# Kernel tuning notes

Hardware: AMD Instinct MI355X
Metric: run time of the kernel (lower is better)

## Reference

```python
import jax, jax.numpy as jnp
import numpy as np

D = 1024
H = 16
HD = D // H
B = 2
S = 2048


def setup_inputs() -> dict:
    key = jax.random.key(0)
    ks = jax.random.split(key, 9)
    sc = 1.0 / np.sqrt(D)
    return {
        "x": jax.random.normal(ks[0], (B, S, D), dtype=jnp.float32),
        "attention_mask": jnp.ones((B, S), dtype=jnp.int32),
        "Wq": jax.random.normal(ks[1], (D, D), dtype=jnp.float32) * sc,
        "bq": jax.random.normal(ks[2], (D,), dtype=jnp.float32) * 0.02,
        "Wk": jax.random.normal(ks[3], (D, D), dtype=jnp.float32) * sc,
        "bk": jax.random.normal(ks[4], (D,), dtype=jnp.float32) * 0.02,
        "Wv": jax.random.normal(ks[5], (D, D), dtype=jnp.float32) * sc,
        "bv": jax.random.normal(ks[6], (D,), dtype=jnp.float32) * 0.02,
        "Wo": jax.random.normal(ks[7], (D, D), dtype=jnp.float32) * sc,
        "bo": jax.random.normal(ks[8], (D,), dtype=jnp.float32) * 0.02,
    }


def reference(x, attention_mask, Wq, bq, Wk, bk, Wv, bv, Wo, bo):
    Bb, Ss, d = x.shape
    # projections (torch Linear: x @ W.T + b; here W stored as [in,out])
    q = (x @ Wq + bq).reshape(Bb, Ss, H, HD).transpose(0, 2, 1, 3)  # [B,H,S,hd]
    k = (x @ Wk + bk).reshape(Bb, Ss, H, HD).transpose(0, 2, 1, 3)
    v = (x @ Wv + bv).reshape(Bb, Ss, H, HD).transpose(0, 2, 1, 3)
    dots = jnp.einsum("bhqd,bhkd->bhqk", q, k) / np.sqrt(HD)  # [B,H,S,S]
    causal = jnp.triu(jnp.ones((Ss, Ss), dtype=bool), k=1)  # True above diagonal
    dots = jnp.where(causal[None, None], -jnp.inf, dots)
    pad = (attention_mask == 0)[:, None, None, :]  # [B,1,1,S]
    dots = jnp.where(pad, -jnp.inf, dots)
    scores = jax.nn.softmax(dots, axis=-1)
    o = jnp.einsum("bhqk,bhkd->bhqd", scores, v)  # [B,H,S,hd]
    o = o.transpose(0, 2, 1, 3).reshape(Bb, Ss, d)
    return o @ Wo + bo
```

## Files before the change

### kernel.cpp

```cpp
#include <hip/hip_runtime.h>

#define D_  1024
#define H_  16
#define HD_ 64
#define B_  2
#define S_  2048
#define M_  (B_*S_)

typedef _Float16 f16;
typedef _Float16 f16x8 __attribute__((ext_vector_type(8)));
typedef _Float16 f16x4 __attribute__((ext_vector_type(4)));
typedef _Float16 f16x2 __attribute__((ext_vector_type(2)));
typedef float    f32x4 __attribute__((ext_vector_type(4)));

#define GLOAD_LDS16(g, l) \
  __builtin_amdgcn_global_load_lds((__attribute__((address_space(1))) const void*)(g), \
                                   (__attribute__((address_space(3))) void*)(l), 16, 0, 0)

__global__ void k_cvt_x(const float* __restrict__ x, f16* __restrict__ xb) {
  int i = blockIdx.x * blockDim.x + threadIdx.x;
  float4 v = ((const float4*)x)[i];
  f16x4 o = { (f16)v.x, (f16)v.y, (f16)v.z, (f16)v.w };
  ((f16x4*)xb)[i] = o;
}

__global__ void k_twt(const float* __restrict__ W, f16* __restrict__ WT) {
  __shared__ float t[32][33];
  int n0 = blockIdx.x * 32, k0 = blockIdx.y * 32;
  int tx = threadIdx.x, ty = threadIdx.y;
  #pragma unroll
  for (int i = 0; i < 4; i++)
    t[ty + i*8][tx] = W[(size_t)(k0 + ty + i*8) * D_ + n0 + tx];
  __syncthreads();
  #pragma unroll
  for (int i = 0; i < 4; i++)
    WT[(size_t)(n0 + ty + i*8) * D_ + k0 + tx] = (f16)t[tx][ty + i*8];
}

template<int MODE>
__device__ __forceinline__ void gemm_body(const f16* __restrict__ A,
                                          const f16* __restrict__ Bt,
                                          const float* __restrict__ bias,
                                          void* __restrict__ Cout) {
  __shared__ __align__(16) f16 lA[128 * 32];
  __shared__ __align__(16) f16 lB[128 * 32];
  const int tid = threadIdx.x;
  const int wv = tid >> 6, lane = tid & 63;
  const int m0 = blockIdx.y * 128, n0 = blockIdx.x * 128;
  const int fr = lane & 15, fg = lane >> 4;
  const int wm = wv >> 1, wn = wv & 1;
  f32x4 acc[4][4] = {};

  for (int k0 = 0; k0 < D_; k0 += 32) {
    #pragma unroll
    for (int it = 0; it < 2; ++it) {
      int c = wv + it * 4;
      int row = c * 16 + (lane >> 2);
      int kk = (lane & 3) * 8;
      GLOAD_LDS16(A  + (size_t)(m0 + row) * D_ + k0 + kk, lA + c * 512);
      GLOAD_LDS16(Bt + (size_t)(n0 + row) * D_ + k0 + kk, lB + c * 512);
    }
    __syncthreads();
    f16x8 a[4], b[4];
    #pragma unroll
    for (int i = 0; i < 4; i++) a[i] = *(const f16x8*)&lA[(wm*64 + i*16 + fr) * 32 + fg * 8];
    #pragma unroll
    for (int j = 0; j < 4; j++) b[j] = *(const f16x8*)&lB[(wn*64 + j*16 + fr) * 32 + fg * 8];
    #pragma unroll
    for (int i = 0; i < 4; i++)
      #pragma unroll
      for (int j = 0; j < 4; j++)
        acc[i][j] = __builtin_amdgcn_mfma_f32_16x16x32_f16(a[i], b[j], acc[i][j], 0, 0, 0);
    __syncthreads();
  }

  #pragma unroll
  for (int i = 0; i < 4; i++) {
    #pragma unroll
    for (int j = 0; j < 4; j++) {
      int grow0 = m0 + wm*64 + i*16 + fg*4;
      int gcol  = n0 + wn*64 + j*16 + fr;
      float bb = bias[gcol];
      #pragma unroll
      for (int r = 0; r < 4; r++) {
        float val = acc[i][j][r] + bb;
        int grow = grow0 + r;
        if (MODE == 0) {
          int b = grow >> 11, s = grow & (S_ - 1);
          int h = gcol >> 6,  hd = gcol & (HD_ - 1);
          ((f16*)Cout)[((size_t)(b * H_ + h) * S_ + s) * HD_ + hd] = (f16)val;
        } else {
          ((float*)Cout)[(size_t)grow * D_ + gcol] = val;
        }
      }
    }
  }
}

__global__ __launch_bounds__(256) void k_gemm_qkv(const f16* __restrict__ A,
                                                  const f16* __restrict__ WT0,
                                                  const float* __restrict__ bq,
                                                  const float* __restrict__ bk,
                                                  const float* __restrict__ bv,
                                                  f16* __restrict__ qkv) {
  int z = blockIdx.z;
  const f16* Bt = WT0 + (size_t)z * D_ * D_;
  const float* bias = (z == 0) ? bq : (z == 1) ? bk : bv;
  f16* outp = qkv + (size_t)z * M_ * D_;
  gemm_body<0>(A, Bt, bias, outp);
}

__global__ __launch_bounds__(256) void k_gemm_out(const f16* __restrict__ A,
                                                  const f16* __restrict__ Bt,
                                                  const float* __restrict__ bias,
                                                  float* __restrict__ Cout) {
  gemm_body<1>(A, Bt, bias, Cout);
}

#define POFF 8.65617025f

__global__ __launch_bounds__(256) void k_attn(const f16* __restrict__ Qh,
                                              const f16* __restrict__ Kh,
                                              const f16* __restrict__ Vh,
                                              const int* __restrict__ am,
                                              f16* __restrict__ OpA, f16* __restrict__ OpB,
                                              float* __restrict__ lpA, float* __restrict__ lpB) {
  __shared__ __align__(16) f16 kt[2][64 * 64];
  __shared__ __align__(16) f16 vt[2][64 * 64];
  __shared__ __align__(16) f16 pl[4][32 * 64];

  const int tid = threadIdx.x;
  const int wv = tid >> 6, lane = tid & 63;
  const int fr = lane & 15, fg = lane >> 4;

  const int d = blockIdx.x;
  const int bh = d & 31;
  const int m  = (d >> 5) & 7;
  const int typeB = d >> 8;
  const int b = bh >> 4, h = bh & 15;
  (void)h;

  f16*   Op = typeB ? OpB : OpA;
  float* lp = typeB ? lpB : lpA;

  const f16* Qb = Qh + (size_t)bh * S_ * HD_;
  const f16* Kb = Kh + (size_t)bh * S_ * HD_;
  const f16* Vb = Vh + (size_t)bh * S_ * HD_;
  const int* amb = am + b * S_;
  f16* plw = pl[wv];

  volatile int* flag = (volatile int*)&pl[0][0];
  if (tid == 0) *flag = 1;
  __syncthreads();
  {
    int mv = 1;
    #pragma unroll
    for (int i = 0; i < 8; ++i) mv &= amb[tid * 8 + i];
    if (!mv) *flag = 0;
  }
  __syncthreads();
  const bool allv = (*flag != 0);

  const f16 qs = (f16)0.18033688f;
  const int ksrc = 8 * ((lane & 7) ^ (lane >> 3));
  const int swz = (fr & 7) << 3;
  const int vkk = (tid >> 3) * 2, vd0 = (tid & 7) * 8;
  const int vswz2 = (tid & 3) << 4;
  const f32x4 cinit = { -POFF, -POFF, -POFF, -POFF };

#define STAGE_K(t_, c_) do { \
    const f16* kp_ = Kb + (size_t)((t_) * 64) * HD_; \
    GLOAD_LDS16(kp_ + (size_t)((wv*2+0)*8 + (lane >> 3)) * HD_ + ksrc, &kt[c_][(wv*2+0)*512]); \
    GLOAD_LDS16(kp_ + (size_t)((wv*2+1)*8 + (lane >> 3)) * HD_ + ksrc, &kt[c_][(wv*2+1)*512]); \
  } while (0)

#define LOAD_V(t_) do { \
    const f16* vp_ = Vb + (size_t)((t_) * 64 + vkk) * HD_ + vd0; \
    vA = *(const f16x8*)vp_; vBr = *(const f16x8*)(vp_ + HD_); \
  } while (0)

#define WRITE_V(c_) do { \
    _Pragma("unroll") \
    for (int j_ = 0; j_ < 8; ++j_) { \
      f16x2 pr_ = { vA[j_], vBr[j_] }; \
      *(f16x2*)&vt[c_][(vd0 + j_) * 64 + ((vkk ^ (j_ << 3)) ^ vswz2)] = pr_; \
    } \
  } while (0)

  f16x8 vA, vBr;

  auto run_half = [&](int qt, int t0, int t1) {
    const int q0w = qt * 128 + wv * 32;

    f16x8 qf[2][2];
    #pragma unroll
    for (int rt = 0; rt < 2; ++rt) {
      f16x8 r0 = *(const f16x8*)&Qb[(size_t)(q0w + rt*16 + fr) * HD_ + fg*8];
      f16x8 r1 = *(const f16x8*)&Qb[(size_t)(q0w + rt*16 + fr) * HD_ + 32 + fg*8];
      qf[rt][0] = r0 * qs; qf[rt][1] = r1 * qs;
    }

    f32x4 accO[2][4] = {};
    float lrl[2] = {0.f, 0.f};

    STAGE_K(t0, 0);
    LOAD_V(t0);
    WRITE_V(0);
    __syncthreads();

    int c = 0;
    for (int t = t0; t < t1; ++t) {
      const int kb = t * 64;
      const bool pre = (t + 1 < t1);
      if (pre) { STAGE_K(t + 1, c ^ 1); LOAD_V(t + 1); }

      const int dq = q0w - kb;
      if (dq + 31 >= 0) {
        int tm1 = (dq + 31) >> 4; if (tm1 > 3) tm1 = 3;
        int tm0 = (dq + 15) >> 4; if (tm0 > 3) tm0 = 3;
        const bool fullb = (dq >= 63);

        f32x4 s[2][4];
        #pragma unroll
        for (int rt = 0; rt < 2; ++rt)
          #pragma unroll
          for (int tt = 0; tt < 4; ++tt) s[rt][tt] = cinit;

        __builtin_amdgcn_s_setprio(1);
        #pragma unroll
        for (int tt = 0; tt < 4; ++tt) {
          if (tt <= tm1) {
            const int kr = (tt*16 + fr) * 64;
            f16x8 kf0 = *(const f16x8*)&kt[c][kr + ((     fg*8) ^ swz)];
            f16x8 kf1 = *(const f16x8*)&kt[c][kr + ((32 + fg*8) ^ swz)];
            s[1][tt] = __builtin_amdgcn_mfma_f32_16x16x32_f16(kf0, qf[1][0], s[1][tt], 0, 0, 0);
            s[1][tt] = __builtin_amdgcn_mfma_f32_16x16x32_f16(kf1, qf[1][1], s[1][tt], 0, 0, 0);
            if (tt <= tm0) {
              s[0][tt] = __builtin_amdgcn_mfma_f32_16x16x32_f16(kf0, qf[0][0], s[0][tt], 0, 0, 0);
              s[0][tt] = __builtin_amdgcn_mfma_f32_16x16x32_f16(kf1, qf[0][1], s[0][tt], 0, 0, 0);
            }
          }
        }
        __builtin_amdgcn_s_setprio(0);

        #pragma unroll
        for (int rt = 0; rt < 2; ++rt) {
          const int tmr = rt ? tm1 : tm0;
          if (tmr < 0) continue;
          const int thr = dq + rt*16 + fr;
          #pragma unroll
          for (int tt = 0; tt < 4; ++tt) {
            f16x4 pk4 = {};
            if (tt <= tmr) {
              if (allv) {
                #pragma unroll
                for (int r = 0; r < 4; ++r) {
                  float sv = s[rt][tt][r];
                  if (!fullb) sv = (tt*16 + fg*4 + r <= thr) ? sv : -1e30f;
                  float p = exp2f(sv);
                  lrl[rt] += p;
                  pk4[r] = (f16)p;
                }
              } else {
                int4 a4 = *(const int4*)&amb[kb + tt*16 + fg*4];
                #pragma unroll
                for (int r = 0; r < 4; ++r) {
                  float sv = s[rt][tt][r];
                  if (!fullb) sv = (tt*16 + fg*4 + r <= thr) ? sv : -1e30f;
                  float p = exp2f(sv);
                  int mr_ = (r == 0) ? a4.x : (r == 1) ? a4.y : (r == 2) ? a4.z : a4.w;
                  p = mr_ ? p : 0.0f;
                  lrl[rt] += p;
                  pk4[r] = (f16)p;
                }
              }
            }
            *(f16x4*)&plw[(rt*16 + fr) * 64 + ((tt*16 + fg*4) ^ swz)] = pk4;
          }
        }

        __builtin_amdgcn_s_setprio(1);
        #pragma unroll
        for (int ks = 0; ks < 2; ++ks) {
          if (ks <= (tm1 >> 1)) {
            f16x8 vf[4];
            #pragma unroll
            for (int nt = 0; nt < 4; ++nt)
              vf[nt] = *(const f16x8*)&vt[c][(nt*16 + fr) * 64 +
                           ((ks*32 + fg*8) ^ swz ^ (((2*nt + (fr >> 3)) & 3) << 4))];
            #pragma unroll
            for (int rt = 0; rt < 2; ++rt) {
              const int tmr = rt ? tm1 : tm0;
              if (tmr >= 0 && ks <= (tmr >> 1)) {
                f16x8 pa = *(const f16x8*)&plw[(rt*16 + fr) * 64 + ((ks*32 + fg*8) ^ swz)];
                #pragma unroll
                for (int nt = 0; nt < 4; ++nt)
                  accO[rt][nt] = __builtin_amdgcn_mfma_f32_16x16x32_f16(pa, vf[nt], accO[rt][nt], 0, 0, 0);
              }
            }
          }
        }
        __builtin_amdgcn_s_setprio(0);
      }

      if (pre) WRITE_V(c ^ 1);
      __syncthreads();
      c ^= 1;
    }

    #pragma unroll
    for (int rt = 0; rt < 2; ++rt) {
      float v = lrl[rt];
      v += __shfl_xor(v, 16);
      v += __shfl_xor(v, 32);
      if (lane < 16) lp[(size_t)bh * S_ + q0w + rt*16 + lane] = v;

      float inv[4];
      (void)inv;
      f16* Oprow = Op + (size_t)bh * (S_ * HD_);
      #pragma unroll
      for (int nt = 0; nt < 4; ++nt) {
        int col = nt*16 + fr;
        #pragma unroll
        for (int r = 0; r < 4; ++r) {
          int row = q0w + rt*16 + fg*4 + r;
          Oprow[(size_t)row * HD_ + col] = (f16)accO[rt][nt][r];
        }
      }
    }
  };

  const int qtA = m, qtB = 15 - m;
  if (!typeB) {
    run_half(qtA, 0, qtA + 1);
    run_half(qtB, 0, qtB + 1);
  } else {
    run_half(qtA, qtA + 1, 2 * (qtA + 1));
    run_half(qtB, qtB + 1, 2 * (qtB + 1));
  }

#undef STAGE_K
#undef LOAD_V
#undef WRITE_V
}

__global__ __launch_bounds__(256) void k_comb(const f16* __restrict__ OA,
                                              const f16* __restrict__ OB,
                                              const float* __restrict__ lA,
                                              const float* __restrict__ lB,
                                              f16* __restrict__ Obf) {
  int gid = blockIdx.x * 256 + threadIdx.x;
  int seg = gid & 7, rowg = gid >> 3;
  int bh = rowg >> 11, row = rowg & 2047;
  f16x8 a  = ((const f16x8*)OA)[gid];
  f16x8 b2 = ((const f16x8*)OB)[gid];
  float inv = __builtin_amdgcn_rcpf(lA[rowg] + lB[rowg]);
  f16x8 o;
  #pragma unroll
  for (int j = 0; j < 8; ++j) o[j] = (f16)(((float)a[j] + (float)b2[j]) * inv);
  int bb = bh >> 4, hh = bh & 15;
  *(f16x8*)&Obf[((size_t)(bb * S_ + row)) * D_ + hh * 64 + seg * 8] = o;
}

extern "C" void kernel_launch(void* const* d_in, const int* in_sizes, int n_in,
                              void* d_out, int out_size, void* d_ws, size_t ws_size,
                              hipStream_t stream) {
  const float* x  = (const float*)d_in[0];
  const int*   am = (const int*)d_in[1];
  const float* Wq = (const float*)d_in[2];
  const float* bq = (const float*)d_in[3];
  const float* Wk = (const float*)d_in[4];
  const float* bk = (const float*)d_in[5];
  const float* Wv = (const float*)d_in[6];
  const float* bv = (const float*)d_in[7];
  const float* Wo = (const float*)d_in[8];
  const float* bo = (const float*)d_in[9];

  char* ws = (char*)d_ws;
  f16*   xb  = (f16*)(ws);
  f16*   wt  = (f16*)(ws + (8u  << 20));
  f16*   qkv = (f16*)(ws + (16u << 20));
  f16*   OpA = (f16*)(ws + (40u << 20));
  f16*   OpB = xb;
  float* lpA = (float*)(ws + (8u << 20));
  float* lpB = (float*)(ws + (8u << 20) + (256u << 10));
  f16*   Obf = qkv;

  k_cvt_x<<<4096, 256, 0, stream>>>(x, xb);

  dim3 tb(32, 8), tg(32, 32);
  k_twt<<<tg, tb, 0, stream>>>(Wq, wt + 0 * (size_t)(D_ * D_));
  k_twt<<<tg, tb, 0, stream>>>(Wk, wt + 1 * (size_t)(D_ * D_));
  k_twt<<<tg, tb, 0, stream>>>(Wv, wt + 2 * (size_t)(D_ * D_));
  k_twt<<<tg, tb, 0, stream>>>(Wo, wt + 3 * (size_t)(D_ * D_));

  k_gemm_qkv<<<dim3(8, 32, 3), 256, 0, stream>>>(xb, wt, bq, bk, bv, qkv);

  k_attn<<<dim3(512), 256, 0, stream>>>(qkv,
                                        qkv + (size_t)M_ * D_,
                                        qkv + 2 * (size_t)M_ * D_,
                                        am, OpA, OpB, lpA, lpB);

  k_comb<<<dim3(2048), 256, 0, stream>>>(OpA, OpB, lpA, lpB, Obf);

  k_gemm_out<<<dim3(8, 32), 256, 0, stream>>>(Obf, wt + 3 * (size_t)(D_ * D_), bo,
                                              (float*)d_out);
}
```

Before: 132.6 us.

## Double-buffer GEMM LDS, merge weight transposes, compute softmax row sums via MFMA

After: 124.6 us. 6.0% less time.

```diff
diff --git a/kernel.cpp b/kernel.cpp
--- a/kernel.cpp
+++ b/kernel.cpp
@@ -11,6 +11,7 @@
 typedef _Float16 f16x8 __attribute__((ext_vector_type(8)));
 typedef _Float16 f16x4 __attribute__((ext_vector_type(4)));
 typedef _Float16 f16x2 __attribute__((ext_vector_type(2)));
+typedef __fp16   h16x2 __attribute__((ext_vector_type(2)));
 typedef float    f32x4 __attribute__((ext_vector_type(4)));
 
 #define GLOAD_LDS16(g, l) \
@@ -24,8 +25,13 @@
   ((f16x4*)xb)[i] = o;
 }
 
-__global__ void k_twt(const float* __restrict__ W, f16* __restrict__ WT) {
+__global__ void k_twt4(const float* __restrict__ Wq, const float* __restrict__ Wk,
+                       const float* __restrict__ Wv, const float* __restrict__ Wo,
+                       f16* __restrict__ WT) {
   __shared__ float t[32][33];
+  int z = blockIdx.z;
+  const float* W = (z == 0) ? Wq : (z == 1) ? Wk : (z == 2) ? Wv : Wo;
+  f16* out = WT + (size_t)z * D_ * D_;
   int n0 = blockIdx.x * 32, k0 = blockIdx.y * 32;
   int tx = threadIdx.x, ty = threadIdx.y;
   #pragma unroll
@@ -34,7 +40,7 @@
   __syncthreads();
   #pragma unroll
   for (int i = 0; i < 4; i++)
-    WT[(size_t)(n0 + ty + i*8) * D_ + k0 + tx] = (f16)t[tx][ty + i*8];
+    out[(size_t)(n0 + ty + i*8) * D_ + k0 + tx] = (f16)t[tx][ty + i*8];
 }
 
 template<int MODE>
@@ -42,37 +48,46 @@
                                           const f16* __restrict__ Bt,
                                           const float* __restrict__ bias,
                                           void* __restrict__ Cout) {
-  __shared__ __align__(16) f16 lA[128 * 32];
-  __shared__ __align__(16) f16 lB[128 * 32];
+  __shared__ __align__(16) f16 lA[2][128 * 32];
+  __shared__ __align__(16) f16 lB[2][128 * 32];
   const int tid = threadIdx.x;
   const int wv = tid >> 6, lane = tid & 63;
   const int m0 = blockIdx.y * 128, n0 = blockIdx.x * 128;
   const int fr = lane & 15, fg = lane >> 4;
   const int wm = wv >> 1, wn = wv & 1;
+  const int srow = (lane >> 2), skk = (lane & 3) * 8;
   f32x4 acc[4][4] = {};
 
+#define G_STAGE(k0_, c_) do { \
+    _Pragma("unroll") \
+    for (int it_ = 0; it_ < 2; ++it_) { \
+      int ch_ = wv + it_ * 4; \
+      int row_ = ch_ * 16 + srow; \
+      GLOAD_LDS16(A  + (size_t)(m0 + row_) * D_ + (k0_) + skk, &lA[c_][ch_ * 512]); \
+      GLOAD_LDS16(Bt + (size_t)(n0 + row_) * D_ + (k0_) + skk, &lB[c_][ch_ * 512]); \
+    } \
+  } while (0)
+
+  G_STAGE(0, 0);
+  __syncthreads();
+
+  int c = 0;
   for (int k0 = 0; k0 < D_; k0 += 32) {
-    #pragma unroll
-    for (int it = 0; it < 2; ++it) {
-      int c = wv + it * 4;
-      int row = c * 16 + (lane >> 2);
-      int kk = (lane & 3) * 8;
-      GLOAD_LDS16(A  + (size_t)(m0 + row) * D_ + k0 + kk, lA + c * 512);
-      GLOAD_LDS16(Bt + (size_t)(n0 + row) * D_ + k0 + kk, lB + c * 512);
-    }
-    __syncthreads();
+    if (k0 + 32 < D_) G_STAGE(k0 + 32, c ^ 1);
     f16x8 a[4], b[4];
     #pragma unroll
-    for (int i = 0; i < 4; i++) a[i] = *(const f16x8*)&lA[(wm*64 + i*16 + fr) * 32 + fg * 8];
-    #pragma unroll
-    for (int j = 0; j < 4; j++) b[j] = *(const f16x8*)&lB[(wn*64 + j*16 + fr) * 32 + fg * 8];
+    for (int i = 0; i < 4; i++) a[i] = *(const f16x8*)&lA[c][(wm*64 + i*16 + fr) * 32 + fg * 8];
+    #pragma unroll
+    for (int j = 0; j < 4; j++) b[j] = *(const f16x8*)&lB[c][(wn*64 + j*16 + fr) * 32 + fg * 8];
     #pragma unroll
     for (int i = 0; i < 4; i++)
       #pragma unroll
       for (int j = 0; j < 4; j++)
         acc[i][j] = __builtin_amdgcn_mfma_f32_16x16x32_f16(a[i], b[j], acc[i][j], 0, 0, 0);
     __syncthreads();
+    c ^= 1;
   }
+#undef G_STAGE
 
   #pragma unroll
   for (int i = 0; i < 4; i++) {
@@ -80,15 +95,17 @@
     for (int j = 0; j < 4; j++) {
       int grow0 = m0 + wm*64 + i*16 + fg*4;
       int gcol  = n0 + wn*64 + j*16 + fr;
-      float bb = bias[gcol];
+      float bb = bias[gcol & (D_ - 1)];
       #pragma unroll
       for (int r = 0; r < 4; r++) {
         float val = acc[i][j][r] + bb;
         int grow = grow0 + r;
         if (MODE == 0) {
+          int z = gcol >> 10, gl = gcol & (D_ - 1);
           int b = grow >> 11, s = grow & (S_ - 1);
-          int h = gcol >> 6,  hd = gcol & (HD_ - 1);
-          ((f16*)Cout)[((size_t)(b * H_ + h) * S_ + s) * HD_ + hd] = (f16)val;
+          int h = gl >> 6,  hd = gl & (HD_ - 1);
+          ((f16*)Cout)[(size_t)z * (M_ * D_) +
+                       ((size_t)(b * H_ + h) * S_ + s) * HD_ + hd] = (f16)val;
         } else {
           ((float*)Cout)[(size_t)grow * D_ + gcol] = val;
         }
@@ -103,11 +120,9 @@
                                                   const float* __restrict__ bk,
                                                   const float* __restrict__ bv,
                                                   f16* __restrict__ qkv) {
-  int z = blockIdx.z;
-  const f16* Bt = WT0 + (size_t)z * D_ * D_;
-  const float* bias = (z == 0) ? bq : (z == 1) ? bk : bv;
-  f16* outp = qkv + (size_t)z * M_ * D_;
-  gemm_body<0>(A, Bt, bias, outp);
+  const int n0 = blockIdx.x * 128;
+  const float* bias = (n0 < 1024) ? bq : (n0 < 2048) ? bk : bv;
+  gemm_body<0>(A, WT0, bias, qkv);
 }
 
 __global__ __launch_bounds__(256) void k_gemm_out(const f16* __restrict__ A,
@@ -167,6 +182,8 @@
   const int vkk = (tid >> 3) * 2, vd0 = (tid & 7) * 8;
   const int vswz2 = (tid & 3) << 4;
   const f32x4 cinit = { -POFF, -POFF, -POFF, -POFF };
+  const f16 one_ = (f16)1.0f;
+  const f16x8 onesf = { one_, one_, one_, one_, one_, one_, one_, one_ };
 
 #define STAGE_K(t_, c_) do { \
     const f16* kp_ = Kb + (size_t)((t_) * 64) * HD_; \
@@ -201,7 +218,7 @@
     }
 
     f32x4 accO[2][4] = {};
-    float lrl[2] = {0.f, 0.f};
+    f32x4 accL[2] = {};
 
     STAGE_K(t0, 0);
     LOAD_V(t0);
@@ -250,16 +267,16 @@
           const int thr = dq + rt*16 + fr;
           #pragma unroll
           for (int tt = 0; tt < 4; ++tt) {
-            f16x4 pk4 = {};
+            union { f16x4 v; h16x2 h[2]; } pk;
+            pk.v = (f16x4){};
             if (tt <= tmr) {
+              float p[4];
               if (allv) {
                 #pragma unroll
                 for (int r = 0; r < 4; ++r) {
                   float sv = s[rt][tt][r];
                   if (!fullb) sv = (tt*16 + fg*4 + r <= thr) ? sv : -1e30f;
-                  float p = exp2f(sv);
-                  lrl[rt] += p;
-                  pk4[r] = (f16)p;
+                  p[r] = exp2f(sv);
                 }
               } else {
                 int4 a4 = *(const int4*)&amb[kb + tt*16 + fg*4];
@@ -267,15 +284,15 @@
                 for (int r = 0; r < 4; ++r) {
                   float sv = s[rt][tt][r];
                   if (!fullb) sv = (tt*16 + fg*4 + r <= thr) ? sv : -1e30f;
-                  float p = exp2f(sv);
+                  float pv = exp2f(sv);
                   int mr_ = (r == 0) ? a4.x : (r == 1) ? a4.y : (r == 2) ? a4.z : a4.w;
-                  p = mr_ ? p : 0.0f;
-                  lrl[rt] += p;
-                  pk4[r] = (f16)p;
+                  p[r] = mr_ ? pv : 0.0f;
                 }
               }
+              pk.h[0] = __builtin_amdgcn_cvt_pkrtz(p[0], p[1]);
+              pk.h[1] = __builtin_amdgcn_cvt_pkrtz(p[2], p[3]);
             }
-            *(f16x4*)&plw[(rt*16 + fr) * 64 + ((tt*16 + fg*4) ^ swz)] = pk4;
+            *(f16x4*)&plw[(rt*16 + fr) * 64 + ((tt*16 + fg*4) ^ swz)] = pk.v;
           }
         }
 
@@ -296,6 +313,7 @@
                 #pragma unroll
                 for (int nt = 0; nt < 4; ++nt)
                   accO[rt][nt] = __builtin_amdgcn_mfma_f32_16x16x32_f16(pa, vf[nt], accO[rt][nt], 0, 0, 0);
+                accL[rt] = __builtin_amdgcn_mfma_f32_16x16x32_f16(pa, onesf, accL[rt], 0, 0, 0);
               }
             }
           }
@@ -310,13 +328,11 @@
 
     #pragma unroll
     for (int rt = 0; rt < 2; ++rt) {
-      float v = lrl[rt];
-      v += __shfl_xor(v, 16);
-      v += __shfl_xor(v, 32);
-      if (lane < 16) lp[(size_t)bh * S_ + q0w + rt*16 + lane] = v;
-
-      float inv[4];
-      (void)inv;
+      if (fr == 0) {
+        #pragma unroll
+        for (int r = 0; r < 4; ++r)
+          lp[(size_t)bh * S_ + q0w + rt*16 + fg*4 + r] = accL[rt][r];
+      }
       f16* Oprow = Op + (size_t)bh * (S_ * HD_);
       #pragma unroll
       for (int nt = 0; nt < 4; ++nt) {
@@ -388,13 +404,10 @@
 
   k_cvt_x<<<4096, 256, 0, stream>>>(x, xb);
 
-  dim3 tb(32, 8), tg(32, 32);
-  k_twt<<<tg, tb, 0, stream>>>(Wq, wt + 0 * (size_t)(D_ * D_));
-  k_twt<<<tg, tb, 0, stream>>>(Wk, wt + 1 * (size_t)(D_ * D_));
-  k_twt<<<tg, tb, 0, stream>>>(Wv, wt + 2 * (size_t)(D_ * D_));
-  k_twt<<<tg, tb, 0, stream>>>(Wo, wt + 3 * (size_t)(D_ * D_));
-
-  k_gemm_qkv<<<dim3(8, 32, 3), 256, 0, stream>>>(xb, wt, bq, bk, bv, qkv);
+  dim3 tb(32, 8), tg4(32, 32, 4);
+  k_twt4<<<tg4, tb, 0, stream>>>(Wq, Wk, Wv, Wo, wt);
+
+  k_gemm_qkv<<<dim3(24, 32), 256, 0, stream>>>(xb, wt, bq, bk, bv, qkv);
 
   k_attn<<<dim3(512), 256, 0, stream>>>(qkv,
                                         qkv + (size_t)M_ * D_,
```
